# Performance work log

Measured on AMD Instinct MI355X. Metric: run time of the kernel, lower is better.

Reference implementation:

```python
import jax, jax.numpy as jnp
import numpy as np

N = 50000
E = 800000
IN_DIM = 512
HID = 512
MLP_HID = 200
N_CLASSES = 2
BN_EPS = 1e-5


def setup_inputs() -> dict:
    key = jax.random.key(0)
    ks = jax.random.split(key, 12)
    def glorot(k, shape):
        fan_in, fan_out = shape[0], shape[1]
        lim = (6.0 / (fan_in + fan_out)) ** 0.5
        return jax.random.uniform(k, shape, jnp.float32, -lim, lim)
    return {
        "features": jax.random.normal(ks[0], (N, IN_DIM), jnp.float32),
        "src": jax.random.randint(ks[1], (E,), 0, N),
        "dst": jax.random.randint(ks[2], (E,), 0, N),
        # SAGEConv layer 1 & 2 (gcn aggregator -> only fc_neigh)
        "W1": glorot(ks[3], (IN_DIM, HID)),
        "b1": jnp.zeros((HID,), jnp.float32),
        "W2": glorot(ks[4], (HID, HID)),
        "b2": jnp.zeros((HID,), jnp.float32),
        # MLP predictor: Linear -> ReLU -> BatchNorm1d -> Linear
        "Wh": glorot(ks[5], (HID, MLP_HID)),
        "bh": jnp.zeros((MLP_HID,), jnp.float32),
        "gamma": jnp.ones((MLP_HID,), jnp.float32),
        "beta": jnp.zeros((MLP_HID,), jnp.float32),
        "Wo": glorot(ks[6], (MLP_HID, N_CLASSES)),
        "bo": jnp.zeros((N_CLASSES,), jnp.float32),
    }


def _sage_gcn_layer(h, src, dst, deg, W, b):
    # dgl.add_self_loop(g) + SAGEConv(aggregator_type='gcn'):
    # neigh_sum over (edges + self-loop) = segment_sum + h;
    # gcn aggregator then adds h_self once more and divides by (in_deg_with_selfloop + 1):
    #   h_neigh = (segment_sum(h[src]) + 2*h) / (deg_orig + 2)
    agg = jax.ops.segment_sum(h[src], dst, num_segments=h.shape[0])
    h_neigh = (agg + 2.0 * h) / (deg + 2.0)[:, None]
    # fc_neigh then activation=relu (fc commutes with the convex aggregation,
    # applied post-aggregation for clarity)
    return jax.nn.relu(h_neigh @ W + b)


def reference(features, src, dst, W1, b1, W2, b2, Wh, bh, gamma, beta, Wo, bo):
    n = features.shape[0]
    deg = jax.ops.segment_sum(jnp.ones_like(src, dtype=features.dtype), dst, num_segments=n)
    h = _sage_gcn_layer(features, src, dst, deg, W1, b1)  # dropout = identity (eval)
    h = _sage_gcn_layer(h, src, dst, deg, W2, b2)
    # MLP predictor (dropout identity): Linear -> ReLU -> BatchNorm1d -> Linear
    h = jax.nn.relu(h @ Wh + bh)
    mean = jnp.mean(h, axis=0)
    var = jnp.var(h, axis=0)  # biased var, matching torch BatchNorm training fwd
    h = (h - mean) * jax.lax.rsqrt(var + BN_EPS) * gamma + beta
    return h @ Wo + bo
```

## Files before the change

kernel.cpp:

```cpp
#include <hip/hip_runtime.h>

#define NN 50000
#define NE 800000
#define DIM 512
#define MLPH 200

typedef __attribute__((ext_vector_type(8))) short short8;
typedef __attribute__((ext_vector_type(4))) float f32x4;
typedef __attribute__((ext_vector_type(4))) unsigned int u32x4;

#define GL2LDS(g, l)                                                     \
    __builtin_amdgcn_global_load_lds(                                    \
        (const __attribute__((address_space(1))) unsigned int*)(g),      \
        (__attribute__((address_space(3))) unsigned int*)(l), 16, 0, 0)

__device__ inline unsigned short f2bf(float f) {
    unsigned int u = __float_as_uint(f);
    unsigned int r = (u + 0x7fffu + ((u >> 16) & 1u)) >> 16;
    return (unsigned short)r;
}
__device__ inline float bflo(unsigned u) { return __uint_as_float(u << 16); }
__device__ inline float bfhi(unsigned u) { return __uint_as_float(u & 0xffff0000u); }
__device__ inline unsigned pack2(float a, float b) {
    return (unsigned)f2bf(a) | ((unsigned)f2bf(b) << 16);
}

__global__ void k_hist(const int* __restrict__ dst, int* __restrict__ counts) {
    int e = blockIdx.x * blockDim.x + threadIdx.x;
    if (e < NE) atomicAdd(&counts[dst[e]], 1);
}

__global__ void k_part(const int* __restrict__ counts, int* __restrict__ partial) {
    int t = threadIdx.x;
    int i = blockIdx.x * 256 + t;
    int x = (i < NN) ? counts[i] : 0;
#pragma unroll
    for (int off = 32; off; off >>= 1) x += __shfl_down(x, off);
    __shared__ int ws[4];
    if ((t & 63) == 0) ws[t >> 6] = x;
    __syncthreads();
    if (t == 0) partial[blockIdx.x] = ws[0] + ws[1] + ws[2] + ws[3];
}

__global__ void k_scanp(int* __restrict__ partial, int* __restrict__ rowstart, int nb) {
    __shared__ int ws[4];
    int t = threadIdx.x;
    int x = (t < nb) ? partial[t] : 0;
    int v = x;
#pragma unroll
    for (int off = 1; off < 64; off <<= 1) {
        int u = __shfl_up(v, off);
        if ((t & 63) >= off) v += u;
    }
    if ((t & 63) == 63) ws[t >> 6] = v;
    __syncthreads();
    int add = 0;
#pragma unroll
    for (int w = 0; w < 4; w++)
        if (w < (t >> 6)) add += ws[w];
    if (t < nb) partial[t] = v - x + add;
    if (t == 255) rowstart[NN] = v + add;
}

__global__ void k_scan2(const int* __restrict__ counts, const int* __restrict__ pexcl,
                        int* __restrict__ rowstart, int* __restrict__ cursor) {
    __shared__ int ws[4];
    int t = threadIdx.x;
    int i = blockIdx.x * 256 + t;
    int x = (i < NN) ? counts[i] : 0;
    int v = x;
#pragma unroll
    for (int off = 1; off < 64; off <<= 1) {
        int u = __shfl_up(v, off);
        if ((t & 63) >= off) v += u;
    }
    if ((t & 63) == 63) ws[t >> 6] = v;
    __syncthreads();
    int add = 0;
#pragma unroll
    for (int w = 0; w < 4; w++)
        if (w < (t >> 6)) add += ws[w];
    if (i < NN) {
        int r = pexcl[blockIdx.x] + v - x + add;
        rowstart[i] = r;
        cursor[i] = r;
    }
}

__global__ void k_fill(const int* __restrict__ src, const int* __restrict__ dst,
                       int* __restrict__ cursor, int* __restrict__ adj) {
    int e = blockIdx.x * blockDim.x + threadIdx.x;
    if (e < NE) {
        int p = atomicAdd(&cursor[dst[e]], 1);
        adj[p] = src[e];
    }
}

__global__ void k_cvt(const float* __restrict__ in, ushort* __restrict__ out, int n4) {
    int i = blockIdx.x * blockDim.x + threadIdx.x;
    if (i >= n4) return;
    float4 v = *(const float4*)(in + (size_t)i * 4);
    ushort2 a{f2bf(v.x), f2bf(v.y)}, b{f2bf(v.z), f2bf(v.w)};
    *(ushort2*)(out + (size_t)i * 4) = a;
    *(ushort2*)(out + (size_t)i * 4 + 2) = b;
}

__global__ void k_wt3(const float* __restrict__ W1, const float* __restrict__ W2,
                      const float* __restrict__ Wh, ushort* __restrict__ W1t,
                      ushort* __restrict__ W2t, ushort* __restrict__ Wht) {
    int i = blockIdx.x * 256 + threadIdx.x;
    const int S1 = 512 * 512, S2 = 2 * 512 * 512, S3 = 2 * 512 * 512 + MLPH * 512;
    if (i < S1) {
        int n = i >> 9, k = i & 511;
        W1t[i] = f2bf(W1[(size_t)k * 512 + n]);
    } else if (i < S2) {
        int j = i - S1, n = j >> 9, k = j & 511;
        W2t[j] = f2bf(W2[(size_t)k * 512 + n]);
    } else if (i < S3) {
        int j = i - S2, n = j >> 9, k = j & 511;
        Wht[j] = f2bf(Wh[(size_t)k * MLPH + n]);
    }
}

__device__ inline void addrow(float* acc, uint4 v) {
    acc[0] += bflo(v.x); acc[1] += bfhi(v.x);
    acc[2] += bflo(v.y); acc[3] += bfhi(v.y);
    acc[4] += bflo(v.z); acc[5] += bfhi(v.z);
    acc[6] += bflo(v.w); acc[7] += bfhi(v.w);
}

__global__ __launch_bounds__(256) void k_agg_bf(const ushort* __restrict__ h,
                                                const int* __restrict__ rowstart,
                                                const int* __restrict__ adj,
                                                ushort* __restrict__ out) {
    int node = blockIdx.x * 4 + (threadIdx.x >> 6);
    int lane = threadIdx.x & 63;
    if (node >= NN) return;
    int s = rowstart[node], e = rowstart[node + 1];
    const size_t coff = (size_t)lane * 8;
    float acc[8];
    {
        uint4 v = *(const uint4*)(h + (size_t)node * DIM + coff);
        acc[0] = 2.f * bflo(v.x); acc[1] = 2.f * bfhi(v.x);
        acc[2] = 2.f * bflo(v.y); acc[3] = 2.f * bfhi(v.y);
        acc[4] = 2.f * bflo(v.z); acc[5] = 2.f * bfhi(v.z);
        acc[6] = 2.f * bflo(v.w); acc[7] = 2.f * bfhi(v.w);
    }
    int i = s;
    int e4 = s + ((e - s) & ~3);
    for (; i < e4; i += 4) {
        int n0 = __builtin_nontemporal_load(adj + i);
        int n1 = __builtin_nontemporal_load(adj + i + 1);
        int n2 = __builtin_nontemporal_load(adj + i + 2);
        int n3 = __builtin_nontemporal_load(adj + i + 3);
        uint4 v0 = *(const uint4*)(h + (size_t)n0 * DIM + coff);
        uint4 v1 = *(const uint4*)(h + (size_t)n1 * DIM + coff);
        uint4 v2 = *(const uint4*)(h + (size_t)n2 * DIM + coff);
        uint4 v3 = *(const uint4*)(h + (size_t)n3 * DIM + coff);
        addrow(acc, v0);
        addrow(acc, v1);
        addrow(acc, v2);
        addrow(acc, v3);
    }
    for (; i < e; i++) {
        int nbr = __builtin_nontemporal_load(adj + i);
        uint4 v = *(const uint4*)(h + (size_t)nbr * DIM + coff);
        addrow(acc, v);
    }
    float inv = 1.0f / (float)(e - s + 2);
    u32x4 o;
    o.x = pack2(acc[0] * inv, acc[1] * inv);
    o.y = pack2(acc[2] * inv, acc[3] * inv);
    o.z = pack2(acc[4] * inv, acc[5] * inv);
    o.w = pack2(acc[6] * inv, acc[7] * inv);
    __builtin_nontemporal_store(o, (u32x4*)(out + (size_t)node * DIM + coff));
}

template <int NCOLS, int OMODE>
__global__ __launch_bounds__(512) void k_ggemm(const ushort* __restrict__ A,
                                               const ushort* __restrict__ Bt,
                                               const float* __restrict__ bias,
                                               float* __restrict__ Cf,
                                               ushort* __restrict__ Cb, int M) {
    constexpr int K = 512;
    constexpr int NT = K / 32;
    constexpr int NC = (NCOLS + 127) / 128;
    __shared__ ushort As[2][256 * 32];
    __shared__ ushort Bs[2][128 * 32];
    const int tid = threadIdx.x;
    const int wid = tid >> 6, lane = tid & 63;
    const int wm = wid >> 1, wn = wid & 1;

    const int cpx = gridDim.x >> 3;
    const int wg = (blockIdx.x & 7) * cpx + (blockIdx.x >> 3);
    const int col0 = (wg % NC) * 128;
    const int row0 = (wg / NC) * 256;

    const int l15 = lane & 15, lk = (lane >> 4) * 8;
    const int lrow = lane >> 2;
    const int lseg = (lane & 3) * 8;

    auto stage = [&](int buf, int k0) {
#pragma unroll
        for (int j = 0; j < 2; j++) {
            const int r = wid * 16 + j * 128;
            int gr = row0 + r + lrow;
            if (gr > M - 1) gr = M - 1;
            GL2LDS(A + (size_t)gr * K + k0 + lseg, &As[buf][r * 32]);
        }
        const int rb = wid * 16;
        int gc = col0 + rb + lrow;
        if (NCOLS % 128 != 0) {
            if (gc > NCOLS - 1) gc = NCOLS - 1;
        }
        GL2LDS(Bt + (size_t)gc * K + k0 + lseg, &Bs[buf][rb * 32]);
    };

    f32x4 acc[4][4] = {};
    stage(0, 0);
    __syncthreads();
    for (int t = 0; t < NT; ++t) {
        const int cur = t & 1;
        if (t + 1 < NT) stage(cur ^ 1, (t + 1) * 32);
        short8 a[4], b[4];
#pragma unroll
        for (int m = 0; m < 4; m++)
            a[m] = *(const short8*)(&As[cur][(wm * 64 + m * 16 + l15) * 32 + lk]);
#pragma unroll
        for (int n = 0; n < 4; n++)
            b[n] = *(const short8*)(&Bs[cur][(wn * 64 + n * 16 + l15) * 32 + lk]);
#pragma unroll
        for (int m = 0; m < 4; m++)
#pragma unroll
            for (int n = 0; n < 4; n++)
                acc[m][n] = __builtin_amdgcn_mfma_f32_16x16x32_bf16(a[m], b[n], acc[m][n], 0, 0, 0);
        __syncthreads();
    }

    const int crow = row0 + wm * 64;
    const int ccol = col0 + wn * 64;
#pragma unroll
    for (int n = 0; n < 4; n++) {
        int c = ccol + n * 16 + l15;
        if (NCOLS % 128 != 0 && c >= NCOLS) continue;
        float bv = bias[c];
#pragma unroll
        for (int m = 0; m < 4; m++) {
#pragma unroll
            for (int i = 0; i < 4; i++) {
                int r = crow + m * 16 + (lane >> 4) * 4 + i;
                if (r >= M) continue;
                float v = fmaxf(acc[m][n][i] + bv, 0.0f);
                if (OMODE == 0) Cf[(size_t)r * NCOLS + c] = v;
                else Cb[(size_t)r * NCOLS + c] = f2bf(v);
            }
        }
    }
}

__global__ void k_bnstat(const float* __restrict__ hm, float* __restrict__ gsum,
                         float* __restrict__ gsq) {
    int j = threadIdx.x;
    if (j >= MLPH) return;
    float s = 0.f, q = 0.f;
    for (int r = blockIdx.x; r < NN; r += gridDim.x) {
        float v = hm[(size_t)r * MLPH + j];
        s += v;
        q += v * v;
    }
    atomicAdd(&gsum[j], s);
    atomicAdd(&gsq[j], q);
}

__global__ void k_bnfin(const float* __restrict__ gsum, const float* __restrict__ gsq,
                        const float* __restrict__ gamma, const float* __restrict__ beta,
                        const float* __restrict__ Wo, const float* __restrict__ bo,
                        float* __restrict__ Wo2, float* __restrict__ bo2) {
    __shared__ float sh[MLPH];
    int j = threadIdx.x;
    if (j < MLPH) {
        float mean = gsum[j] / (float)NN;
        float var = gsq[j] / (float)NN - mean * mean;
        float scale = gamma[j] * rsqrtf(var + 1e-5f);
        float shift = beta[j] - mean * scale;
        sh[j] = shift;
        Wo2[j * 2 + 0] = scale * Wo[j * 2 + 0];
        Wo2[j * 2 + 1] = scale * Wo[j * 2 + 1];
    }
    __syncthreads();
    if (j < 2) {
        float acc = bo[j];
        for (int t = 0; t < MLPH; t++) acc += sh[t] * Wo[t * 2 + j];
        bo2[j] = acc;
    }
}

__global__ void k_out(const float* __restrict__ hm, const float* __restrict__ Wo2,
                      const float* __restrict__ bo2, float* __restrict__ out) {
    __shared__ float w[MLPH * 2];
    if (threadIdx.x < MLPH * 2) w[threadIdx.x] = Wo2[threadIdx.x];
    __syncthreads();
    int wid = (blockIdx.x * blockDim.x + threadIdx.x) >> 6;
    int lane = threadIdx.x & 63;
    if (wid >= NN) return;
    const float* row = hm + (size_t)wid * MLPH;
    float p0 = 0.f, p1 = 0.f;
    for (int j = lane; j < MLPH; j += 64) {
        float v = row[j];
        p0 += v * w[j * 2 + 0];
        p1 += v * w[j * 2 + 1];
    }
    for (int off = 32; off; off >>= 1) {
        p0 += __shfl_down(p0, off);
        p1 += __shfl_down(p1, off);
    }
    if (lane == 0) {
        out[wid * 2 + 0] = p0 + bo2[0];
        out[wid * 2 + 1] = p1 + bo2[1];
    }
}

extern "C" void kernel_launch(void* const* d_in, const int* in_sizes, int n_in,
                              void* d_out, int out_size, void* d_ws, size_t ws_size,
                              hipStream_t stream) {
    const float* features = (const float*)d_in[0];
    const int* src = (const int*)d_in[1];
    const int* dst = (const int*)d_in[2];
    const float* W1 = (const float*)d_in[3];
    const float* b1 = (const float*)d_in[4];
    const float* W2 = (const float*)d_in[5];
    const float* b2 = (const float*)d_in[6];
    const float* Wh = (const float*)d_in[7];
    const float* bh = (const float*)d_in[8];
    const float* gamma = (const float*)d_in[9];
    const float* beta = (const float*)d_in[10];
    const float* Wo = (const float*)d_in[11];
    const float* bo = (const float*)d_in[12];
    float* out = (float*)d_out;

    char* w = (char*)d_ws;
    auto alloc = [&](size_t bytes) -> void* {
        void* p = (void*)w;
        w += (bytes + 255) & ~(size_t)255;
        return p;
    };
    ushort* fb = (ushort*)alloc((size_t)NN * DIM * 2);
    ushort* ab = (ushort*)alloc((size_t)NN * DIM * 2);
    ushort* hb = (ushort*)alloc((size_t)NN * DIM * 2);
    float* hm = (float*)alloc((size_t)NN * MLPH * 4);
    ushort* W1t = (ushort*)alloc((size_t)DIM * DIM * 2);
    ushort* W2t = (ushort*)alloc((size_t)DIM * DIM * 2);
    ushort* Wht = (ushort*)alloc((size_t)MLPH * DIM * 2);
    int* adj = (int*)alloc((size_t)NE * 4);
    int* counts = (int*)alloc((size_t)NN * 4);
    int* rowstart = (int*)alloc((size_t)(NN + 1) * 4);
    int* cursor = (int*)alloc((size_t)NN * 4);
    int* partial = (int*)alloc(256 * 4);
    float* gsum = (float*)alloc(MLPH * 4);
    float* gsq = (float*)alloc(MLPH * 4);
    float* Wo2 = (float*)alloc(MLPH * 2 * 4);
    float* bo2 = (float*)alloc(2 * 4);

    hipMemsetAsync(counts, 0, (size_t)NN * 4, stream);
    hipMemsetAsync(gsum, 0, MLPH * 4, stream);
    hipMemsetAsync(gsq, 0, MLPH * 4, stream);

    const int NB = (NN + 255) / 256;

    k_hist<<<(NE + 255) / 256, 256, 0, stream>>>(dst, counts);
    k_part<<<NB, 256, 0, stream>>>(counts, partial);
    k_scanp<<<1, 256, 0, stream>>>(partial, rowstart, NB);
    k_scan2<<<NB, 256, 0, stream>>>(counts, partial, rowstart, cursor);
    k_fill<<<(NE + 255) / 256, 256, 0, stream>>>(src, dst, cursor, adj);

    const int n4 = NN * DIM / 4;
    k_cvt<<<(n4 + 255) / 256, 256, 0, stream>>>(features, fb, n4);
    const int WT = 2 * 512 * 512 + MLPH * 512;
    k_wt3<<<(WT + 255) / 256, 256, 0, stream>>>(W1, W2, Wh, W1t, W2t, Wht);

    const int MBr = (NN + 255) / 256;
    const int G512 = 4 * MBr;
    const int G200 = 2 * MBr;

    k_agg_bf<<<(NN + 3) / 4, 256, 0, stream>>>(fb, rowstart, adj, ab);
    k_ggemm<DIM, 1><<<G512, 512, 0, stream>>>(ab, W1t, b1, nullptr, hb, NN);
    k_agg_bf<<<(NN + 3) / 4, 256, 0, stream>>>(hb, rowstart, adj, ab);
    k_ggemm<DIM, 1><<<G512, 512, 0, stream>>>(ab, W2t, b2, nullptr, fb, NN);
    k_ggemm<MLPH, 0><<<G200, 512, 0, stream>>>(fb, Wht, bh, hm, nullptr, NN);
    k_bnstat<<<512, 256, 0, stream>>>(hm, gsum, gsq);
    k_bnfin<<<1, 256, 0, stream>>>(gsum, gsq, gamma, beta, Wo, bo, Wo2, bo2);
    k_out<<<(NN * 64 + 511) / 512, 512, 0, stream>>>(hm, Wo2, bo2, out);
}
```

Baseline: 595.6 us.

## Triple-buffer GEMM LDS staging, store MLP hidden as bf16, drop nontemporal adj loads

```diff
diff --git a/kernel.cpp b/kernel.cpp
--- a/kernel.cpp
+++ b/kernel.cpp
@@ -21,6 +21,7 @@
 }
 __device__ inline float bflo(unsigned u) { return __uint_as_float(u << 16); }
 __device__ inline float bfhi(unsigned u) { return __uint_as_float(u & 0xffff0000u); }
+__device__ inline float bf1(unsigned short u) { return __uint_as_float((unsigned)u << 16); }
 __device__ inline unsigned pack2(float a, float b) {
     return (unsigned)f2bf(a) | ((unsigned)f2bf(b) << 16);
 }
@@ -149,10 +150,7 @@
     int i = s;
     int e4 = s + ((e - s) & ~3);
     for (; i < e4; i += 4) {
-        int n0 = __builtin_nontemporal_load(adj + i);
-        int n1 = __builtin_nontemporal_load(adj + i + 1);
-        int n2 = __builtin_nontemporal_load(adj + i + 2);
-        int n3 = __builtin_nontemporal_load(adj + i + 3);
+        int n0 = adj[i], n1 = adj[i + 1], n2 = adj[i + 2], n3 = adj[i + 3];
         uint4 v0 = *(const uint4*)(h + (size_t)n0 * DIM + coff);
         uint4 v1 = *(const uint4*)(h + (size_t)n1 * DIM + coff);
         uint4 v2 = *(const uint4*)(h + (size_t)n2 * DIM + coff);
@@ -163,7 +161,7 @@
         addrow(acc, v3);
     }
     for (; i < e; i++) {
-        int nbr = __builtin_nontemporal_load(adj + i);
+        int nbr = adj[i];
         uint4 v = *(const uint4*)(h + (size_t)nbr * DIM + coff);
         addrow(acc, v);
     }
@@ -185,8 +183,8 @@
     constexpr int K = 512;
     constexpr int NT = K / 32;
     constexpr int NC = (NCOLS + 127) / 128;
-    __shared__ ushort As[2][256 * 32];
-    __shared__ ushort Bs[2][128 * 32];
+    __shared__ ushort As[3][256 * 32];
+    __shared__ ushort Bs[3][128 * 32];
     const int tid = threadIdx.x;
     const int wid = tid >> 6, lane = tid & 63;
     const int wm = wid >> 1, wn = wid & 1;
@@ -218,10 +216,13 @@
 
     f32x4 acc[4][4] = {};
     stage(0, 0);
-    __syncthreads();
+    stage(1, 32);
+    asm volatile("s_waitcnt vmcnt(3)" ::: "memory");
+    __builtin_amdgcn_s_barrier();
+
     for (int t = 0; t < NT; ++t) {
-        const int cur = t & 1;
-        if (t + 1 < NT) stage(cur ^ 1, (t + 1) * 32);
+        const int cur = t % 3;
+        if (t + 2 < NT) stage((t + 2) % 3, (t + 2) * 32);
         short8 a[4], b[4];
 #pragma unroll
         for (int m = 0; m < 4; m++)
@@ -234,7 +235,13 @@
 #pragma unroll
             for (int n = 0; n < 4; n++)
                 acc[m][n] = __builtin_amdgcn_mfma_f32_16x16x32_bf16(a[m], b[n], acc[m][n], 0, 0, 0);
-        __syncthreads();
+        if (t + 2 < NT) {
+            asm volatile("s_waitcnt vmcnt(3)" ::: "memory");
+            __builtin_amdgcn_s_barrier();
+        } else if (t + 1 < NT) {
+            asm volatile("s_waitcnt vmcnt(0)" ::: "memory");
+            __builtin_amdgcn_s_barrier();
+        }
     }
 
     const int crow = row0 + wm * 64;
@@ -258,13 +265,13 @@
     }
 }
 
-__global__ void k_bnstat(const float* __restrict__ hm, float* __restrict__ gsum,
+__global__ void k_bnstat(const ushort* __restrict__ hm, float* __restrict__ gsum,
                          float* __restrict__ gsq) {
     int j = threadIdx.x;
     if (j >= MLPH) return;
     float s = 0.f, q = 0.f;
     for (int r = blockIdx.x; r < NN; r += gridDim.x) {
-        float v = hm[(size_t)r * MLPH + j];
+        float v = bf1(hm[(size_t)r * MLPH + j]);
         s += v;
         q += v * v;
     }
@@ -295,7 +302,7 @@
     }
 }
 
-__global__ void k_out(const float* __restrict__ hm, const float* __restrict__ Wo2,
+__global__ void k_out(const ushort* __restrict__ hm, const float* __restrict__ Wo2,
                       const float* __restrict__ bo2, float* __restrict__ out) {
     __shared__ float w[MLPH * 2];
     if (threadIdx.x < MLPH * 2) w[threadIdx.x] = Wo2[threadIdx.x];
@@ -303,10 +310,10 @@
     int wid = (blockIdx.x * blockDim.x + threadIdx.x) >> 6;
     int lane = threadIdx.x & 63;
     if (wid >= NN) return;
-    const float* row = hm + (size_t)wid * MLPH;
+    const ushort* row = hm + (size_t)wid * MLPH;
     float p0 = 0.f, p1 = 0.f;
     for (int j = lane; j < MLPH; j += 64) {
-        float v = row[j];
+        float v = bf1(row[j]);
         p0 += v * w[j * 2 + 0];
         p1 += v * w[j * 2 + 1];
     }
@@ -347,7 +354,6 @@
     ushort* fb = (ushort*)alloc((size_t)NN * DIM * 2);
     ushort* ab = (ushort*)alloc((size_t)NN * DIM * 2);
     ushort* hb = (ushort*)alloc((size_t)NN * DIM * 2);
-    float* hm = (float*)alloc((size_t)NN * MLPH * 4);
     ushort* W1t = (ushort*)alloc((size_t)DIM * DIM * 2);
     ushort* W2t = (ushort*)alloc((size_t)DIM * DIM * 2);
     ushort* Wht = (ushort*)alloc((size_t)MLPH * DIM * 2);
@@ -386,8 +392,8 @@
     k_ggemm<DIM, 1><<<G512, 512, 0, stream>>>(ab, W1t, b1, nullptr, hb, NN);
     k_agg_bf<<<(NN + 3) / 4, 256, 0, stream>>>(hb, rowstart, adj, ab);
     k_ggemm<DIM, 1><<<G512, 512, 0, stream>>>(ab, W2t, b2, nullptr, fb, NN);
-    k_ggemm<MLPH, 0><<<G200, 512, 0, stream>>>(fb, Wht, bh, hm, nullptr, NN);
-    k_bnstat<<<512, 256, 0, stream>>>(hm, gsum, gsq);
+    k_ggemm<MLPH, 1><<<G200, 512, 0, stream>>>(fb, Wht, bh, nullptr, ab, NN);
+    k_bnstat<<<512, 256, 0, stream>>>(ab, gsum, gsq);
     k_bnfin<<<1, 256, 0, stream>>>(gsum, gsq, gamma, beta, Wo, bo, Wo2, bo2);
-    k_out<<<(NN * 64 + 511) / 512, 512, 0, stream>>>(hm, Wo2, bo2, out);
-}
+    k_out<<<(NN * 64 + 511) / 512, 512, 0, stream>>>(ab, Wo2, bo2, out);
+}
```

Measured after the change: 591.4 us, median of 2. About the same (-0.7%).
